# Optimization experiments

Measured on AMD Instinct MI355X. Metric: run time of the kernel, lower is better.

Reference implementation:

```python
import jax, jax.numpy as jnp
import numpy as np

N_NODES = 100000
N_EDGES = 1600000
F_IN = 64
HID = 64
N_CLASSES = 45
N_GRAPHS = 256


def gcn_conv(x, src, dst, W, b, n):
    # GCNConv with added self-loops and symmetric normalization (PyG semantics)
    h = x @ W  # [N, H]
    deg = jax.ops.segment_sum(jnp.ones(src.shape[0], h.dtype), dst, num_segments=n) + 1.0
    dinv = jax.lax.rsqrt(deg)  # deg^{-1/2}, deg >= 1 due to self loops
    coef = dinv[src] * dinv[dst]  # [E]
    msg = h[src] * coef[:, None]  # gather + scale
    agg = jax.ops.segment_sum(msg, dst, num_segments=n)  # scatter-add to dst
    agg = agg + h * (dinv * dinv)[:, None]  # self-loop contribution
    return agg + b


def setup_inputs() -> dict:
    key = jax.random.key(0)
    ks = jax.random.split(key, 12)
    x = jax.random.normal(ks[0], (N_NODES, F_IN), dtype=jnp.float32)
    edge_index = jax.random.randint(ks[1], (2, N_EDGES), 0, N_NODES, dtype=jnp.int32)
    batch = jnp.sort(jax.random.randint(ks[2], (N_NODES,), 0, N_GRAPHS, dtype=jnp.int32))
    s1 = 1.0 / np.sqrt(F_IN)
    s2 = 1.0 / np.sqrt(HID)
    W1 = jax.random.uniform(ks[3], (F_IN, HID), jnp.float32, -s1, s1)
    b1 = jnp.zeros((HID,), jnp.float32)
    W2 = jax.random.uniform(ks[4], (HID, HID), jnp.float32, -s2, s2)
    b2 = jnp.zeros((HID,), jnp.float32)
    W3 = jax.random.uniform(ks[5], (HID, HID), jnp.float32, -s2, s2)
    b3 = jnp.zeros((HID,), jnp.float32)
    Wl = jax.random.uniform(ks[6], (HID, N_CLASSES), jnp.float32, -s2, s2)
    bl = jnp.zeros((N_CLASSES,), jnp.float32)
    return {"x": x, "edge_index": edge_index, "batch": batch,
            "W1": W1, "b1": b1, "W2": W2, "b2": b2, "W3": W3, "b3": b3,
            "Wl": Wl, "bl": bl}


def reference(x, edge_index, batch, W1, b1, W2, b2, W3, b3, Wl, bl):
    n = x.shape[0]
    src, dst = edge_index[0], edge_index[1]
    h = jax.nn.relu(gcn_conv(x, src, dst, W1, b1, n))
    h = jax.nn.relu(gcn_conv(h, src, dst, W2, b2, n))
    h = gcn_conv(h, src, dst, W3, b3, n)
    # global mean pool over graph segments
    sums = jax.ops.segment_sum(h, batch, num_segments=N_GRAPHS)  # [G, H]
    cnts = jax.ops.segment_sum(jnp.ones(n, h.dtype), batch, num_segments=N_GRAPHS)
    pooled = sums / jnp.maximum(cnts, 1.0)[:, None]
    # dropout is identity in eval mode
    return pooled @ Wl + bl  # [G, num_classes]
```

## Files before the change

### kernel.cpp

```cpp
#include <hip/hip_runtime.h>
#include <hip/hip_bf16.h>

#define N_NODES   100000
#define N_EDGES   1600000
#define F_IN      64
#define HID       64
#define N_CLASSES 45
#define N_GRAPHS  256
#define SB        392
#define NPB       256
#define CAP       4608
#define WPB       72
#define CHUNK     4096
#define NCHUNK    391
#define NZB       192
#define GEMM_GRID 3125
#define AGGE_GRID 7056
#define NZB2      192
#define ZLEN4_F   1600000
#define ZLEN4_A   1604096

__device__ __forceinline__ float rl_f(float v, int k) {
    return __uint_as_float(__builtin_amdgcn_readlane(__float_as_uint(v), k));
}
__device__ __forceinline__ int rl_i(int v, int k) {
    return __builtin_amdgcn_readlane(v, k);
}
__device__ __forceinline__ unsigned short f2bf(float x) {
    unsigned u = __float_as_uint(x);
    unsigned r = u + 0x7FFFu + ((u >> 16) & 1u);
    return (unsigned short)(r >> 16);
}
__device__ __forceinline__ float bf2f(unsigned short h) {
    return __uint_as_float(((unsigned)h) << 16);
}

__global__ __launch_bounds__(256) void k_front(const int* __restrict__ src, const int* __restrict__ dst,
                                               int* __restrict__ bcur, int* __restrict__ binned,
                                               const float* __restrict__ x, const float* __restrict__ W1,
                                               unsigned short* __restrict__ P, float* __restrict__ zbase) {
    int bid = blockIdx.x;
    int t   = threadIdx.x;
    if (bid < NCHUNK) {
        __shared__ int stg[CHUNK];
        __shared__ unsigned short bkt[CHUNK];
        __shared__ int h[512], cur[512], off[512];
        __shared__ int ps[256];
        h[t] = 0; h[t + 256] = 0;
        __syncthreads();
        int base4 = bid * (CHUNK / 4);
        #pragma unroll
        for (int i = 0; i < CHUNK / 1024; i++) {
            int e4 = base4 + i * 256 + t;
            if (e4 < N_EDGES / 4) {
                int4 d = ((const int4*)dst)[e4];
                atomicAdd(&h[d.x >> 8], 1);
                atomicAdd(&h[d.y >> 8], 1);
                atomicAdd(&h[d.z >> 8], 1);
                atomicAdd(&h[d.w >> 8], 1);
            }
        }
        __syncthreads();
        int a0 = h[2 * t], a1 = h[2 * t + 1];
        ps[t] = a0 + a1;
        __syncthreads();
        for (int o = 1; o < 256; o <<= 1) {
            int v = (t >= o) ? ps[t - o] : 0;
            __syncthreads();
            if (t >= o) ps[t] += v;
            __syncthreads();
        }
        int pex = ps[t] - (a0 + a1);
        int e0 = pex, e1 = pex + a0;
        cur[2 * t] = e0; cur[2 * t + 1] = e1;
        if (2 * t < SB && a0 > 0)
            off[2 * t] = (2 * t) * CAP + atomicAdd(&bcur[2 * t], a0) - e0;
        if (2 * t + 1 < SB && a1 > 0)
            off[2 * t + 1] = (2 * t + 1) * CAP + atomicAdd(&bcur[2 * t + 1], a1) - e1;
        __syncthreads();
        int total = ps[255];
        #pragma unroll
        for (int i = 0; i < CHUNK / 1024; i++) {
            int e4 = base4 + i * 256 + t;
            if (e4 < N_EDGES / 4) {
                int4 d  = ((const int4*)dst)[e4];
                int4 s4 = ((const int4*)src)[e4];
                int q;
                q = atomicAdd(&cur[d.x >> 8], 1); stg[q] = s4.x | ((d.x & 255) << 17); bkt[q] = (unsigned short)(d.x >> 8);
                q = atomicAdd(&cur[d.y >> 8], 1); stg[q] = s4.y | ((d.y & 255) << 17); bkt[q] = (unsigned short)(d.y >> 8);
                q = atomicAdd(&cur[d.z >> 8], 1); stg[q] = s4.z | ((d.z & 255) << 17); bkt[q] = (unsigned short)(d.z >> 8);
                q = atomicAdd(&cur[d.w >> 8], 1); stg[q] = s4.w | ((d.w & 255) << 17); bkt[q] = (unsigned short)(d.w >> 8);
            }
        }
        __syncthreads();
        for (int i = t; i < total; i += 256) {
            int b = bkt[i];
            binned[off[b] + i] = stg[i];
        }
    } else if (bid < NCHUNK + NZB) {
        float4 z = make_float4(0.f, 0.f, 0.f, 0.f);
        float4* zp = (float4*)zbase;
        int zb = bid - NCHUNK;
        for (long i = (long)zb * 256 + t; i < (long)ZLEN4_F; i += (long)NZB * 256)
            zp[i] = z;
    } else {
        int gbid = bid - NCHUNK - NZB;
        int lane = t & 63;
        int wv   = t >> 6;
        int base = gbid * 32 + wv * 8;
        float xr[8], acc[8];
        #pragma unroll
        for (int r = 0; r < 8; r++) {
            xr[r]  = x[(size_t)(base + r) * 64 + lane];
            acc[r] = 0.f;
        }
        for (int kb = 0; kb < 64; kb += 8) {
            float wb[8];
            #pragma unroll
            for (int j = 0; j < 8; j++) wb[j] = W1[(kb + j) * 64 + lane];
            #pragma unroll
            for (int j = 0; j < 8; j++) {
                #pragma unroll
                for (int r = 0; r < 8; r++)
                    acc[r] = fmaf(rl_f(xr[r], kb + j), wb[j], acc[r]);
            }
        }
        #pragma unroll
        for (int r = 0; r < 8; r++)
            P[(size_t)(base + r) * 64 + lane] = f2bf(acc[r]);
    }
}

__global__ __launch_bounds__(256) void k_bcsr(const int* __restrict__ binned, const int* __restrict__ bcur,
                                              float* __restrict__ dinv, float* __restrict__ dinv2,
                                              int* __restrict__ csr) {
    __shared__ int h[NPB];
    __shared__ int ts[NPB];
    int t = threadIdx.x;
    int b = blockIdx.x;
    int nb0  = b << 8;
    int ebeg = b * CAP;
    int ecnt = bcur[b]; if (ecnt > CAP) ecnt = CAP;
    h[t] = 0;
    __syncthreads();
    for (int i = t; i < ecnt; i += 256)
        atomicAdd(&h[binned[ebeg + i] >> 17], 1);
    __syncthreads();
    int c = h[t];
    ts[t] = c;
    __syncthreads();
    for (int o = 1; o < 256; o <<= 1) {
        int v = (t >= o) ? ts[t - o] : 0;
        __syncthreads();
        if (t >= o) ts[t] += v;
        __syncthreads();
    }
    int excl = ts[t] - c + ebeg;
    int n = nb0 + t;
    if (n < N_NODES) {
        float inv = 1.0f / (float)(c + 1);
        dinv2[n] = inv;
        dinv[n]  = sqrtf(inv);
    }
    __syncthreads();
    h[t] = excl;
    __syncthreads();
    for (int i = t; i < ecnt; i += 256) {
        int p = binned[ebeg + i];
        int q = atomicAdd(&h[p >> 17], 1);
        csr[q] = p;
    }
}

template<bool POOLI>
__global__ __launch_bounds__(256) void k_gemm(const float* __restrict__ E,
                                              unsigned short* P,
                                              const float* __restrict__ W,
                                              const float* __restrict__ bprev,
                                              const float* __restrict__ bcurr,
                                              const float* __restrict__ dinv2,
                                              const int* __restrict__ batch,
                                              float* __restrict__ pool) {
    int lane = threadIdx.x & 63;
    int wv   = threadIdx.x >> 6;
    int base = blockIdx.x * 32 + wv * 8;
    float bp = bprev[lane];
    float xr[8], acc[8];
    #pragma unroll
    for (int r = 0; r < 8; r++) {
        int n = base + r;
        float hp = bf2f(P[(size_t)n * 64 + lane]);
        float a  = E[(size_t)n * 64 + lane] + fmaf(hp, dinv2[n], bp);
        xr[r]  = fmaxf(a, 0.f);
        acc[r] = 0.f;
    }
    for (int kb = 0; kb < 64; kb += 8) {
        float wb[8];
        #pragma unroll
        for (int j = 0; j < 8; j++) wb[j] = W[(kb + j) * 64 + lane];
        #pragma unroll
        for (int j = 0; j < 8; j++) {
            #pragma unroll
            for (int r = 0; r < 8; r++)
                acc[r] = fmaf(rl_f(xr[r], kb + j), wb[j], acc[r]);
        }
    }
    #pragma unroll
    for (int r = 0; r < 8; r++)
        P[(size_t)(base + r) * 64 + lane] = f2bf(acc[r]);
    if (POOLI) {
        float bv = bcurr[lane];
        float d2[8];
        #pragma unroll
        for (int r = 0; r < 8; r++) d2[r] = dinv2[base + r];
        int g0 = batch[base], g7 = batch[base + 7];
        if (g0 == g7) {
            float s = 0.f;
            #pragma unroll
            for (int r = 0; r < 8; r++) s += fmaf(acc[r], d2[r], bv);
            atomicAdd(&pool[g0 * 64 + lane], s);
        } else {
            #pragma unroll
            for (int r = 0; r < 8; r++) {
                int g = batch[base + r];
                atomicAdd(&pool[g * 64 + lane], fmaf(acc[r], d2[r], bv));
            }
        }
    }
}

template<bool POOLEP, bool ZROLE>
__global__ __launch_bounds__(256, 8) void k_agge(const unsigned short* __restrict__ Hbuf,
                                                 const int* __restrict__ csr,
                                                 const int* __restrict__ bcur,
                                                 const float* __restrict__ dinv,
                                                 const int* __restrict__ batch,
                                                 float* __restrict__ Out,
                                                 float* __restrict__ zbase) {
    int t = threadIdx.x;
    if (ZROLE && blockIdx.x >= AGGE_GRID) {
        float4 z = make_float4(0.f, 0.f, 0.f, 0.f);
        float4* zp = (float4*)zbase;
        int zb = blockIdx.x - AGGE_GRID;
        for (long i = (long)zb * 256 + t; i < (long)ZLEN4_A; i += (long)NZB2 * 256)
            zp[i] = z;
        return;
    }
    int wv   = t >> 6;
    int lane = t & 63;
    int wid  = blockIdx.x * 4 + wv;
    int b    = wid / WPB;
    int lw   = wid - b * WPB;
    int used = bcur[b]; if (used > CAP) used = CAP;
    int e0   = lw * 64;
    int rem  = used - e0;
    if (rem <= 0) return;
    if (rem > 64) rem = 64;
    int base = b * CAP + e0;

    int p = 0;
    float cv = 0.f;
    if (lane < rem) {
        p  = csr[base + lane];
        cv = dinv[p & 0x1FFFF];
    }
    int sv = p & 0x1FFFF;
    int dv = p >> 17;

    auto flush = [&](int dl, float a) {
        int dst = (b << 8) + dl;
        if (dst < N_NODES) {
            float val = dinv[dst] * a;
            if (POOLEP) {
                int g = batch[dst];
                atomicAdd(&Out[g * 64 + lane], val);
            } else {
                atomicAdd(&Out[(size_t)dst * 64 + lane], val);
            }
        }
    };

    int dprev = rl_i(dv, 0);
    float acc = 0.f;
    int j = 0;
    for (; j + 16 <= rem; j += 16) {
        unsigned short u[16];
        #pragma unroll
        for (int i = 0; i < 16; i++) {
            int s = rl_i(sv, j + i);
            u[i] = Hbuf[(size_t)s * 64 + lane];
        }
        #pragma unroll
        for (int i = 0; i < 16; i++) {
            int   d = rl_i(dv, j + i);
            float c = rl_f(cv, j + i);
            if (d != dprev) { flush(dprev, acc); acc = 0.f; dprev = d; }
            acc = fmaf(bf2f(u[i]), c, acc);
        }
    }
    for (; j < rem; j++) {
        int   s0 = rl_i(sv, j);
        float c0 = rl_f(cv, j);
        int   d0 = rl_i(dv, j);
        unsigned short u0 = Hbuf[(size_t)s0 * 64 + lane];
        if (d0 != dprev) { flush(dprev, acc); acc = 0.f; dprev = d0; }
        acc = fmaf(bf2f(u0), c0, acc);
    }
    flush(dprev, acc);
}

__device__ __forceinline__ int lbound(const int* __restrict__ a, int n, int v) {
    int lo = 0, hi = n;
    while (lo < hi) { int m = (lo + hi) >> 1; if (a[m] < v) lo = m + 1; else hi = m; }
    return lo;
}

__global__ __launch_bounds__(64) void k_cls(const float* __restrict__ pool, const int* __restrict__ batch,
                                            const float* __restrict__ Wl, const float* __restrict__ bl,
                                            float* __restrict__ out) {
    __shared__ float pm[64];
    __shared__ int bounds[2];
    int g = blockIdx.x;
    int t = threadIdx.x;
    if (t < 2) bounds[t] = lbound(batch, N_NODES, g + t);
    __syncthreads();
    float cnt = (float)(bounds[1] - bounds[0]);
    pm[t] = pool[g * 64 + t] / fmaxf(cnt, 1.0f);
    __syncthreads();
    if (t < N_CLASSES) {
        float o = bl[t];
        #pragma unroll
        for (int k = 0; k < HID; k++) o = fmaf(pm[k], Wl[k * N_CLASSES + t], o);
        out[g * N_CLASSES + t] = o;
    }
}


extern "C" void kernel_launch(void* const* d_in, const int* in_sizes, int n_in,
                              void* d_out, int out_size, void* d_ws, size_t ws_size,
                              hipStream_t stream) {
    const float* x     = (const float*)d_in[0];
    const int*   eidx  = (const int*)  d_in[1];
    const int*   batch = (const int*)  d_in[2];
    const float* W1 = (const float*)d_in[3];
    const float* b1 = (const float*)d_in[4];
    const float* W2 = (const float*)d_in[5];
    const float* b2 = (const float*)d_in[6];
    const float* W3 = (const float*)d_in[7];
    const float* b3 = (const float*)d_in[8];
    const float* Wl = (const float*)d_in[9];
    const float* bl = (const float*)d_in[10];
    const int* src = eidx;
    const int* dst = eidx + N_EDGES;

    char* p = (char*)d_ws;
    auto alloc = [&](size_t bytes) -> void* {
        void* r = (void*)p;
        p += (bytes + 255) & ~(size_t)255;
        return r;
    };
    float* dinv  = (float*)alloc((size_t)N_NODES * 4);
    float* dinv2 = (float*)alloc((size_t)N_NODES * 4);
    int*   csr   = (int*)  alloc((size_t)SB * CAP * 4);
    unsigned short* P = (unsigned short*)alloc((size_t)N_NODES * 64 * 2);
    float* E1    = (float*)alloc((size_t)N_NODES * 64 * 4);
    float* pool  = (float*)alloc((size_t)N_GRAPHS * 64 * 4);
    float* E2    = (float*)alloc((size_t)N_NODES * 64 * 4);
    int*   bcur  = (int*)  alloc((size_t)SB * 4);
    int*   binned = (int*) alloc((size_t)SB * CAP * 4);

    const int front_grid = NCHUNK + NZB + GEMM_GRID;

    hipMemsetAsync(bcur, 0, (size_t)SB * 4, stream);
    k_front<<<front_grid, 256, 0, stream>>>(src, dst, bcur, binned, x, W1, P, E1);
    k_bcsr <<<SB, 256, 0, stream>>>(binned, bcur, dinv, dinv2, csr);

    k_agge<false, true ><<<AGGE_GRID + NZB2, 256, 0, stream>>>(P, csr, bcur, dinv, batch, E1, pool);
    k_gemm<false><<<GEMM_GRID, 256, 0, stream>>>(E1, P, W2, b1, nullptr, dinv2, batch, nullptr);
    k_agge<false, false><<<AGGE_GRID, 256, 0, stream>>>(P, csr, bcur, dinv, batch, E2, nullptr);
    k_gemm<true ><<<GEMM_GRID, 256, 0, stream>>>(E2, P, W3, b2, b3, dinv2, batch, pool);
    k_agge<true , false><<<AGGE_GRID, 256, 0, stream>>>(P, csr, bcur, dinv, batch, pool, nullptr);

    k_cls<<<N_GRAPHS, 64, 0, stream>>>(pool, batch, Wl, bl, (float*)d_out);
}
```

Before: 368.7 us.

## Aggregate edges in shared memory per half-bucket and write outputs directly

The edge aggregation kernel now assigns each 512-thread block half of a 256-node destination bucket and accumulates messages into a 128x64 LDS tile with shared atomics. It then writes the scaled rows straight to the output, or reduces them per graph for pooling. This removes the global zero-fill passes for E1/E2 and the per-destination global float atomics, and the zeroing blocks in k_front are dropped. The cost is more LDS use per block and fewer, larger blocks (782), which may lower occupancy and balance work less evenly.

```diff
diff --git a/kernel.cpp b/kernel.cpp
--- a/kernel.cpp
+++ b/kernel.cpp
@@ -8,17 +8,12 @@
 #define N_CLASSES 45
 #define N_GRAPHS  256
 #define SB        392
-#define NPB       256
+#define NB        391
+#define NHB       782
 #define CAP       4608
-#define WPB       72
 #define CHUNK     4096
 #define NCHUNK    391
-#define NZB       192
 #define GEMM_GRID 3125
-#define AGGE_GRID 7056
-#define NZB2      192
-#define ZLEN4_F   1600000
-#define ZLEN4_A   1604096
 
 __device__ __forceinline__ float rl_f(float v, int k) {
     return __uint_as_float(__builtin_amdgcn_readlane(__float_as_uint(v), k));
@@ -38,7 +33,7 @@
 __global__ __launch_bounds__(256) void k_front(const int* __restrict__ src, const int* __restrict__ dst,
                                                int* __restrict__ bcur, int* __restrict__ binned,
                                                const float* __restrict__ x, const float* __restrict__ W1,
-                                               unsigned short* __restrict__ P, float* __restrict__ zbase) {
+                                               unsigned short* __restrict__ P) {
     int bid = blockIdx.x;
     int t   = threadIdx.x;
     if (bid < NCHUNK) {
@@ -97,14 +92,8 @@
             int b = bkt[i];
             binned[off[b] + i] = stg[i];
         }
-    } else if (bid < NCHUNK + NZB) {
-        float4 z = make_float4(0.f, 0.f, 0.f, 0.f);
-        float4* zp = (float4*)zbase;
-        int zb = bid - NCHUNK;
-        for (long i = (long)zb * 256 + t; i < (long)ZLEN4_F; i += (long)NZB * 256)
-            zp[i] = z;
     } else {
-        int gbid = bid - NCHUNK - NZB;
+        int gbid = bid - NCHUNK;
         int lane = t & 63;
         int wv   = t >> 6;
         int base = gbid * 32 + wv * 8;
@@ -133,9 +122,9 @@
 
 __global__ __launch_bounds__(256) void k_bcsr(const int* __restrict__ binned, const int* __restrict__ bcur,
                                               float* __restrict__ dinv, float* __restrict__ dinv2,
-                                              int* __restrict__ csr) {
-    __shared__ int h[NPB];
-    __shared__ int ts[NPB];
+                                              int* __restrict__ csr, int* __restrict__ hb) {
+    __shared__ int h[256];
+    __shared__ int ts[256];
     int t = threadIdx.x;
     int b = blockIdx.x;
     int nb0  = b << 8;
@@ -156,6 +145,7 @@
         __syncthreads();
     }
     int excl = ts[t] - c + ebeg;
+    if (t == 128) hb[b] = excl;
     int n = nb0 + t;
     if (n < N_NODES) {
         float inv = 1.0f / (float)(c + 1);
@@ -229,84 +219,106 @@
     }
 }
 
-template<bool POOLEP, bool ZROLE>
-__global__ __launch_bounds__(256, 8) void k_agge(const unsigned short* __restrict__ Hbuf,
+template<bool POOLEP>
+__global__ __launch_bounds__(512, 8) void k_agge(const unsigned short* __restrict__ Hbuf,
                                                  const int* __restrict__ csr,
                                                  const int* __restrict__ bcur,
+                                                 const int* __restrict__ hb,
                                                  const float* __restrict__ dinv,
                                                  const int* __restrict__ batch,
-                                                 float* __restrict__ Out,
-                                                 float* __restrict__ zbase) {
+                                                 float* __restrict__ Out) {
+    __shared__ float accs[128 * 64];
     int t = threadIdx.x;
-    if (ZROLE && blockIdx.x >= AGGE_GRID) {
+    {
         float4 z = make_float4(0.f, 0.f, 0.f, 0.f);
-        float4* zp = (float4*)zbase;
-        int zb = blockIdx.x - AGGE_GRID;
-        for (long i = (long)zb * 256 + t; i < (long)ZLEN4_A; i += (long)NZB2 * 256)
-            zp[i] = z;
-        return;
-    }
-    int wv   = t >> 6;
-    int lane = t & 63;
-    int wid  = blockIdx.x * 4 + wv;
-    int b    = wid / WPB;
-    int lw   = wid - b * WPB;
-    int used = bcur[b]; if (used > CAP) used = CAP;
-    int e0   = lw * 64;
-    int rem  = used - e0;
-    if (rem <= 0) return;
-    if (rem > 64) rem = 64;
-    int base = b * CAP + e0;
-
-    int p = 0;
-    float cv = 0.f;
-    if (lane < rem) {
-        p  = csr[base + lane];
-        cv = dinv[p & 0x1FFFF];
-    }
-    int sv = p & 0x1FFFF;
-    int dv = p >> 17;
-
-    auto flush = [&](int dl, float a) {
-        int dst = (b << 8) + dl;
-        if (dst < N_NODES) {
-            float val = dinv[dst] * a;
-            if (POOLEP) {
-                int g = batch[dst];
-                atomicAdd(&Out[g * 64 + lane], val);
-            } else {
-                atomicAdd(&Out[(size_t)dst * 64 + lane], val);
-            }
-        }
-    };
-
-    int dprev = rl_i(dv, 0);
-    float acc = 0.f;
-    int j = 0;
-    for (; j + 16 <= rem; j += 16) {
-        unsigned short u[16];
-        #pragma unroll
-        for (int i = 0; i < 16; i++) {
-            int s = rl_i(sv, j + i);
-            u[i] = Hbuf[(size_t)s * 64 + lane];
-        }
-        #pragma unroll
-        for (int i = 0; i < 16; i++) {
-            int   d = rl_i(dv, j + i);
-            float c = rl_f(cv, j + i);
-            if (d != dprev) { flush(dprev, acc); acc = 0.f; dprev = d; }
-            acc = fmaf(bf2f(u[i]), c, acc);
-        }
-    }
-    for (; j < rem; j++) {
-        int   s0 = rl_i(sv, j);
-        float c0 = rl_f(cv, j);
-        int   d0 = rl_i(dv, j);
-        unsigned short u0 = Hbuf[(size_t)s0 * 64 + lane];
-        if (d0 != dprev) { flush(dprev, acc); acc = 0.f; dprev = d0; }
-        acc = fmaf(bf2f(u0), c0, acc);
-    }
-    flush(dprev, acc);
+        #pragma unroll
+        for (int i = 0; i < 4; i++) ((float4*)accs)[t + 512 * i] = z;
+    }
+    int blk  = blockIdx.x;
+    int b    = blk >> 1;
+    int half = blk & 1;
+    int ebeg = b * CAP;
+    int ecnt = bcur[b]; if (ecnt > CAP) ecnt = CAP;
+    int hs   = half ? hb[b] : ebeg;
+    int he   = half ? (ebeg + ecnt) : hb[b];
+    __syncthreads();
+
+    int wv = t >> 6, lane = t & 63;
+    int cnt   = he - hs;
+    int chunk = (cnt + 7) >> 3;
+    int cs = hs + wv * chunk;
+    int ce = cs + chunk; if (ce > he) ce = he;
+    if (cs < ce) {
+        int dprev = -1;
+        float acc = 0.f;
+        for (int base = cs; base < ce; base += 64) {
+            int rem = ce - base; if (rem > 64) rem = 64;
+            int p = 0; float cv = 0.f;
+            if (lane < rem) {
+                p  = csr[base + lane];
+                cv = dinv[p & 0x1FFFF];
+            }
+            int sv = p & 0x1FFFF;
+            int dv = (p >> 17) & 127;
+            if (dprev < 0) dprev = rl_i(dv, 0);
+            int j = 0;
+            for (; j + 16 <= rem; j += 16) {
+                unsigned short u[16];
+                #pragma unroll
+                for (int i = 0; i < 16; i++) {
+                    int s = rl_i(sv, j + i);
+                    u[i] = Hbuf[(size_t)s * 64 + lane];
+                }
+                #pragma unroll
+                for (int i = 0; i < 16; i++) {
+                    int   d = rl_i(dv, j + i);
+                    float c = rl_f(cv, j + i);
+                    if (d != dprev) { atomicAdd(&accs[dprev * 64 + lane], acc); acc = 0.f; dprev = d; }
+                    acc = fmaf(bf2f(u[i]), c, acc);
+                }
+            }
+            for (; j < rem; j++) {
+                int   s0 = rl_i(sv, j);
+                float c0 = rl_f(cv, j);
+                int   d0 = rl_i(dv, j);
+                unsigned short u0 = Hbuf[(size_t)s0 * 64 + lane];
+                if (d0 != dprev) { atomicAdd(&accs[dprev * 64 + lane], acc); acc = 0.f; dprev = d0; }
+                acc = fmaf(bf2f(u0), c0, acc);
+            }
+        }
+        if (dprev >= 0) atomicAdd(&accs[dprev * 64 + lane], acc);
+    }
+    __syncthreads();
+
+    int nb0 = (b << 8) + half * 128;
+    if (!POOLEP) {
+        #pragma unroll
+        for (int i = 0; i < 4; i++) {
+            int f = t + 512 * i;
+            int r = f >> 4;
+            int n = nb0 + r;
+            if (n < N_NODES) {
+                float dn = dinv[n];
+                float4 v = ((float4*)accs)[f];
+                v.x *= dn; v.y *= dn; v.z *= dn; v.w *= dn;
+                ((float4*)Out)[(size_t)n * 16 + (f & 15)] = v;
+            }
+        }
+    } else {
+        float ga = 0.f; int gprev = -1;
+        int r0 = wv * 16;
+        for (int r = r0; r < r0 + 16; r++) {
+            int n = nb0 + r;
+            if (n >= N_NODES) break;
+            int g = batch[n];
+            if (g != gprev) {
+                if (gprev >= 0) atomicAdd(&Out[gprev * 64 + lane], ga);
+                ga = 0.f; gprev = g;
+            }
+            ga = fmaf(accs[r * 64 + lane], dinv[n], ga);
+        }
+        if (gprev >= 0) atomicAdd(&Out[gprev * 64 + lane], ga);
+    }
 }
 
 __device__ __forceinline__ int lbound(const int* __restrict__ a, int n, int v) {
@@ -368,18 +380,18 @@
     float* E2    = (float*)alloc((size_t)N_NODES * 64 * 4);
     int*   bcur  = (int*)  alloc((size_t)SB * 4);
     int*   binned = (int*) alloc((size_t)SB * CAP * 4);
-
-    const int front_grid = NCHUNK + NZB + GEMM_GRID;
+    int*   hb    = (int*)  alloc((size_t)NB * 4);
 
     hipMemsetAsync(bcur, 0, (size_t)SB * 4, stream);
-    k_front<<<front_grid, 256, 0, stream>>>(src, dst, bcur, binned, x, W1, P, E1);
-    k_bcsr <<<SB, 256, 0, stream>>>(binned, bcur, dinv, dinv2, csr);
-
-    k_agge<false, true ><<<AGGE_GRID + NZB2, 256, 0, stream>>>(P, csr, bcur, dinv, batch, E1, pool);
+    hipMemsetAsync(pool, 0, (size_t)N_GRAPHS * 64 * 4, stream);
+    k_front<<<NCHUNK + GEMM_GRID, 256, 0, stream>>>(src, dst, bcur, binned, x, W1, P);
+    k_bcsr <<<NB, 256, 0, stream>>>(binned, bcur, dinv, dinv2, csr, hb);
+
+    k_agge<false><<<NHB, 512, 0, stream>>>(P, csr, bcur, hb, dinv, batch, E1);
     k_gemm<false><<<GEMM_GRID, 256, 0, stream>>>(E1, P, W2, b1, nullptr, dinv2, batch, nullptr);
-    k_agge<false, false><<<AGGE_GRID, 256, 0, stream>>>(P, csr, bcur, dinv, batch, E2, nullptr);
+    k_agge<false><<<NHB, 512, 0, stream>>>(P, csr, bcur, hb, dinv, batch, E2);
     k_gemm<true ><<<GEMM_GRID, 256, 0, stream>>>(E2, P, W3, b2, b3, dinv2, batch, pool);
-    k_agge<true , false><<<AGGE_GRID, 256, 0, stream>>>(P, csr, bcur, dinv, batch, pool, nullptr);
+    k_agge<true ><<<NHB, 512, 0, stream>>>(P, csr, bcur, hb, dinv, batch, pool);
 
     k_cls<<<N_GRAPHS, 64, 0, stream>>>(pool, batch, Wl, bl, (float*)d_out);
 }
```

Result: slower. 441.0 us (+19.6%).

## Split wave into quarter-waves each gathering four features per lane over edge subsets

Applied to the files above, without the earlier changes.

The aggregation kernel now has each 16-lane quarter-wave walk its own 16 edges, and each lane loads 8 bytes (four bf16 features) per edge. Edge indices and coefficients are broadcast with ds_bpermute instead of readlane. Before, one lane handled one feature and every lane looped serially over all 64 edges. The goal is wider gathers and a shorter serial dependency chain per lane, at the cost of more segment boundaries and so more atomic adds. Padded lanes push zero-valued atomics to node b<<8.

```diff
diff --git a/kernel.cpp b/kernel.cpp
--- a/kernel.cpp
+++ b/kernel.cpp
@@ -258,55 +258,69 @@
     if (rem > 64) rem = 64;
     int base = b * CAP + e0;
 
-    int p = 0;
-    float cv = 0.f;
+    int ql = lane & 15;
+    int qw = lane >> 4;
+    int fb = ql * 8;
+
+    int p = 0; float cv = 0.f;
     if (lane < rem) {
         p  = csr[base + lane];
         cv = dinv[p & 0x1FFFF];
     }
-    int sv = p & 0x1FFFF;
-    int dv = p >> 17;
-
-    auto flush = [&](int dl, float a) {
-        int dst = (b << 8) + dl;
+    int cvi = __float_as_int(cv);
+    int ai0 = qw * 64;
+
+    float a0 = 0.f, a1 = 0.f, a2 = 0.f, a3 = 0.f;
+    int dprev = -1;
+
+    auto flush4 = [&]() {
+        int dst = (b << 8) + dprev;
         if (dst < N_NODES) {
-            float val = dinv[dst] * a;
-            if (POOLEP) {
-                int g = batch[dst];
-                atomicAdd(&Out[g * 64 + lane], val);
-            } else {
-                atomicAdd(&Out[(size_t)dst * 64 + lane], val);
-            }
+            float dn = dinv[dst];
+            float* o;
+            if (POOLEP) o = &Out[(size_t)batch[dst] * 64 + ql * 4];
+            else        o = &Out[(size_t)dst * 64 + ql * 4];
+            atomicAdd(o + 0, dn * a0);
+            atomicAdd(o + 1, dn * a1);
+            atomicAdd(o + 2, dn * a2);
+            atomicAdd(o + 3, dn * a3);
         }
     };
 
-    int dprev = rl_i(dv, 0);
-    float acc = 0.f;
-    int j = 0;
-    for (; j + 16 <= rem; j += 16) {
-        unsigned short u[16];
-        #pragma unroll
-        for (int i = 0; i < 16; i++) {
-            int s = rl_i(sv, j + i);
-            u[i] = Hbuf[(size_t)s * 64 + lane];
-        }
-        #pragma unroll
-        for (int i = 0; i < 16; i++) {
-            int   d = rl_i(dv, j + i);
-            float c = rl_f(cv, j + i);
-            if (d != dprev) { flush(dprev, acc); acc = 0.f; dprev = d; }
-            acc = fmaf(bf2f(u[i]), c, acc);
-        }
-    }
-    for (; j < rem; j++) {
-        int   s0 = rl_i(sv, j);
-        float c0 = rl_f(cv, j);
-        int   d0 = rl_i(dv, j);
-        unsigned short u0 = Hbuf[(size_t)s0 * 64 + lane];
-        if (d0 != dprev) { flush(dprev, acc); acc = 0.f; dprev = d0; }
-        acc = fmaf(bf2f(u0), c0, acc);
-    }
-    flush(dprev, acc);
+    #pragma unroll
+    for (int hh = 0; hh < 2; hh++) {
+        int pm[8], cm[8];
+        #pragma unroll
+        for (int i = 0; i < 8; i++) {
+            pm[i] = __builtin_amdgcn_ds_bpermute(ai0 + (hh * 8 + i) * 4, p);
+            cm[i] = __builtin_amdgcn_ds_bpermute(ai0 + (hh * 8 + i) * 4, cvi);
+        }
+        uint2 u[8];
+        #pragma unroll
+        for (int i = 0; i < 8; i++) {
+            unsigned voff = ((unsigned)(pm[i] & 0x1FFFF) << 7) + (unsigned)fb;
+            u[i] = *(const uint2*)((const char*)Hbuf + voff);
+        }
+        #pragma unroll
+        for (int i = 0; i < 8; i++) {
+            int   d = pm[i] >> 17;
+            float c = __int_as_float(cm[i]);
+            if (d != dprev) {
+                if (dprev >= 0) flush4();
+                a0 = a1 = a2 = a3 = 0.f;
+                dprev = d;
+            }
+            float f0 = __uint_as_float(u[i].x << 16);
+            float f1 = __uint_as_float(u[i].x & 0xFFFF0000u);
+            float f2 = __uint_as_float(u[i].y << 16);
+            float f3 = __uint_as_float(u[i].y & 0xFFFF0000u);
+            a0 = fmaf(f0, c, a0);
+            a1 = fmaf(f1, c, a1);
+            a2 = fmaf(f2, c, a2);
+            a3 = fmaf(f3, c, a3);
+        }
+    }
+    if (dprev >= 0) flush4();
 }
 
 __device__ __forceinline__ int lbound(const int* __restrict__ a, int n, int v) {
```

Measured after the change: 911.9 us. 147% more time.

## Switch edge-parallel aggregation to node-per-wave CSR gather with direct stores

Applied to the files above, without the earlier changes.

The aggregation kernel now assigns one wavefront per destination node, using a packed row-pointer/degree array built in the CSR pass. Each node accumulates its neighbours in registers and writes its output row once, instead of segmenting 64-edge chunks and flushing with global atomics. This removes the per-edge atomics and the zero-fill passes for the E1/E2 buffers, since outputs are now fully overwritten. The cost is load imbalance from varying degree and idle lanes for low-degree nodes. Degrees are clamped at 2047 in the packed encoding.

```diff
diff --git a/kernel.cpp b/kernel.cpp
--- a/kernel.cpp
+++ b/kernel.cpp
@@ -10,15 +10,10 @@
 #define SB        392
 #define NPB       256
 #define CAP       4608
-#define WPB       72
 #define CHUNK     4096
 #define NCHUNK    391
-#define NZB       192
 #define GEMM_GRID 3125
-#define AGGE_GRID 7056
-#define NZB2      192
-#define ZLEN4_F   1600000
-#define ZLEN4_A   1604096
+#define AGG_GRID  25000
 
 __device__ __forceinline__ float rl_f(float v, int k) {
     return __uint_as_float(__builtin_amdgcn_readlane(__float_as_uint(v), k));
@@ -38,7 +33,7 @@
 __global__ __launch_bounds__(256) void k_front(const int* __restrict__ src, const int* __restrict__ dst,
                                                int* __restrict__ bcur, int* __restrict__ binned,
                                                const float* __restrict__ x, const float* __restrict__ W1,
-                                               unsigned short* __restrict__ P, float* __restrict__ zbase) {
+                                               unsigned short* __restrict__ P) {
     int bid = blockIdx.x;
     int t   = threadIdx.x;
     if (bid < NCHUNK) {
@@ -97,14 +92,8 @@
             int b = bkt[i];
             binned[off[b] + i] = stg[i];
         }
-    } else if (bid < NCHUNK + NZB) {
-        float4 z = make_float4(0.f, 0.f, 0.f, 0.f);
-        float4* zp = (float4*)zbase;
-        int zb = bid - NCHUNK;
-        for (long i = (long)zb * 256 + t; i < (long)ZLEN4_F; i += (long)NZB * 256)
-            zp[i] = z;
     } else {
-        int gbid = bid - NCHUNK - NZB;
+        int gbid = bid - NCHUNK;
         int lane = t & 63;
         int wv   = t >> 6;
         int base = gbid * 32 + wv * 8;
@@ -133,7 +122,7 @@
 
 __global__ __launch_bounds__(256) void k_bcsr(const int* __restrict__ binned, const int* __restrict__ bcur,
                                               float* __restrict__ dinv, float* __restrict__ dinv2,
-                                              int* __restrict__ csr) {
+                                              int* __restrict__ csr, unsigned* __restrict__ rpd) {
     __shared__ int h[NPB];
     __shared__ int ts[NPB];
     int t = threadIdx.x;
@@ -161,6 +150,8 @@
         float inv = 1.0f / (float)(c + 1);
         dinv2[n] = inv;
         dinv[n]  = sqrtf(inv);
+        int cc = c > 2047 ? 2047 : c;
+        rpd[n] = (unsigned)excl | ((unsigned)cc << 21);
     }
     __syncthreads();
     h[t] = excl;
@@ -229,84 +220,48 @@
     }
 }
 
-template<bool POOLEP, bool ZROLE>
+template<bool POOLEP>
 __global__ __launch_bounds__(256, 8) void k_agge(const unsigned short* __restrict__ Hbuf,
                                                  const int* __restrict__ csr,
-                                                 const int* __restrict__ bcur,
+                                                 const unsigned* __restrict__ rpd,
                                                  const float* __restrict__ dinv,
                                                  const int* __restrict__ batch,
-                                                 float* __restrict__ Out,
-                                                 float* __restrict__ zbase) {
-    int t = threadIdx.x;
-    if (ZROLE && blockIdx.x >= AGGE_GRID) {
-        float4 z = make_float4(0.f, 0.f, 0.f, 0.f);
-        float4* zp = (float4*)zbase;
-        int zb = blockIdx.x - AGGE_GRID;
-        for (long i = (long)zb * 256 + t; i < (long)ZLEN4_A; i += (long)NZB2 * 256)
-            zp[i] = z;
-        return;
-    }
+                                                 float* __restrict__ Out) {
+    int t    = threadIdx.x;
     int wv   = t >> 6;
     int lane = t & 63;
-    int wid  = blockIdx.x * 4 + wv;
-    int b    = wid / WPB;
-    int lw   = wid - b * WPB;
-    int used = bcur[b]; if (used > CAP) used = CAP;
-    int e0   = lw * 64;
-    int rem  = used - e0;
-    if (rem <= 0) return;
-    if (rem > 64) rem = 64;
-    int base = b * CAP + e0;
-
-    int p = 0;
-    float cv = 0.f;
-    if (lane < rem) {
-        p  = csr[base + lane];
-        cv = dinv[p & 0x1FFFF];
-    }
-    int sv = p & 0x1FFFF;
-    int dv = p >> 17;
-
-    auto flush = [&](int dl, float a) {
-        int dst = (b << 8) + dl;
-        if (dst < N_NODES) {
-            float val = dinv[dst] * a;
-            if (POOLEP) {
-                int g = batch[dst];
-                atomicAdd(&Out[g * 64 + lane], val);
-            } else {
-                atomicAdd(&Out[(size_t)dst * 64 + lane], val);
-            }
-        }
-    };
-
-    int dprev = rl_i(dv, 0);
+    int n    = blockIdx.x * 4 + wv;
+    unsigned pd = rpd[n];
+    int rp  = (int)(pd & 0x1FFFFFu);
+    int deg = (int)(pd >> 21);
+
     float acc = 0.f;
-    int j = 0;
-    for (; j + 16 <= rem; j += 16) {
-        unsigned short u[16];
-        #pragma unroll
-        for (int i = 0; i < 16; i++) {
-            int s = rl_i(sv, j + i);
-            u[i] = Hbuf[(size_t)s * 64 + lane];
-        }
-        #pragma unroll
-        for (int i = 0; i < 16; i++) {
-            int   d = rl_i(dv, j + i);
-            float c = rl_f(cv, j + i);
-            if (d != dprev) { flush(dprev, acc); acc = 0.f; dprev = d; }
-            acc = fmaf(bf2f(u[i]), c, acc);
-        }
-    }
-    for (; j < rem; j++) {
-        int   s0 = rl_i(sv, j);
-        float c0 = rl_f(cv, j);
-        int   d0 = rl_i(dv, j);
-        unsigned short u0 = Hbuf[(size_t)s0 * 64 + lane];
-        if (d0 != dprev) { flush(dprev, acc); acc = 0.f; dprev = d0; }
-        acc = fmaf(bf2f(u0), c0, acc);
-    }
-    flush(dprev, acc);
+    for (int e0 = 0; e0 < deg; e0 += 64) {
+        int rem = deg - e0; if (rem > 64) rem = 64;
+        int p = 0; float cv = 0.f;
+        if (lane < rem) {
+            p  = csr[rp + e0 + lane];
+            cv = dinv[p & 0x1FFFF];
+        }
+        int nb = (rem + 15) >> 4;
+        for (int bb = 0; bb < nb; bb++) {
+            unsigned short u[16];
+            #pragma unroll
+            for (int i = 0; i < 16; i++) {
+                unsigned s = (unsigned)(rl_i(p, bb * 16 + i) & 0x1FFFF);
+                u[i] = Hbuf[((size_t)s << 6) + lane];
+            }
+            #pragma unroll
+            for (int i = 0; i < 16; i++)
+                acc = fmaf(bf2f(u[i]), rl_f(cv, bb * 16 + i), acc);
+        }
+    }
+    float val = dinv[n] * acc;
+    if (POOLEP) {
+        atomicAdd(&Out[(size_t)batch[n] * 64 + lane], val);
+    } else {
+        Out[(size_t)n * 64 + lane] = val;
+    }
 }
 
 __device__ __forceinline__ int lbound(const int* __restrict__ a, int n, int v) {
@@ -368,18 +323,18 @@
     float* E2    = (float*)alloc((size_t)N_NODES * 64 * 4);
     int*   bcur  = (int*)  alloc((size_t)SB * 4);
     int*   binned = (int*) alloc((size_t)SB * CAP * 4);
-
-    const int front_grid = NCHUNK + NZB + GEMM_GRID;
+    unsigned* rpd = (unsigned*)alloc((size_t)(SB * NPB) * 4);
 
     hipMemsetAsync(bcur, 0, (size_t)SB * 4, stream);
-    k_front<<<front_grid, 256, 0, stream>>>(src, dst, bcur, binned, x, W1, P, E1);
-    k_bcsr <<<SB, 256, 0, stream>>>(binned, bcur, dinv, dinv2, csr);
-
-    k_agge<false, true ><<<AGGE_GRID + NZB2, 256, 0, stream>>>(P, csr, bcur, dinv, batch, E1, pool);
+    hipMemsetAsync(pool, 0, (size_t)N_GRAPHS * 64 * 4, stream);
+    k_front<<<NCHUNK + GEMM_GRID, 256, 0, stream>>>(src, dst, bcur, binned, x, W1, P);
+    k_bcsr <<<SB, 256, 0, stream>>>(binned, bcur, dinv, dinv2, csr, rpd);
+
+    k_agge<false><<<AGG_GRID, 256, 0, stream>>>(P, csr, rpd, dinv, batch, E1);
     k_gemm<false><<<GEMM_GRID, 256, 0, stream>>>(E1, P, W2, b1, nullptr, dinv2, batch, nullptr);
-    k_agge<false, false><<<AGGE_GRID, 256, 0, stream>>>(P, csr, bcur, dinv, batch, E2, nullptr);
+    k_agge<false><<<AGG_GRID, 256, 0, stream>>>(P, csr, rpd, dinv, batch, E2);
     k_gemm<true ><<<GEMM_GRID, 256, 0, stream>>>(E2, P, W3, b2, b3, dinv2, batch, pool);
-    k_agge<true , false><<<AGGE_GRID, 256, 0, stream>>>(P, csr, bcur, dinv, batch, pool, nullptr);
+    k_agge<true ><<<AGG_GRID, 256, 0, stream>>>(P, csr, rpd, dinv, batch, pool);
 
     k_cls<<<N_GRAPHS, 64, 0, stream>>>(pool, batch, Wl, bl, (float*)d_out);
 }
```

Result: slower. 390.3 us (+5.9%).
